# Performance work log

Measured on AMD Instinct MI355X. Metric: run time of the kernel, lower is better.

Reference implementation:

```python
import jax, jax.numpy as jnp
import numpy as np

V, H, TS, TT, B, PAD = 32000, 512, 48, 48, 64, 0


def setup_inputs() -> dict:
    key = jax.random.key(0)
    ks = jax.random.split(key, 26)
    s = 0.02
    rn = lambda k, shape: (jax.random.normal(k, shape, jnp.float32) * s)
    emb = rn(ks[0], (V, H)).at[PAD].set(0.0)  # padding_idx row zeroed
    return dict(
        src=jax.random.randint(ks[1], (TS, B), 0, V),
        tgt=jax.random.randint(ks[2], (TT, B), 0, V),
        emb=emb,
        enc0_Wih=rn(ks[3], (3 * H, H)), enc0_bih=rn(ks[4], (3 * H,)),
        enc0_Ur=rn(ks[5], (H, H)), enc0_Uz=rn(ks[6], (H, H)),
        enc0_Un=rn(ks[7], (H, H)), enc0_bn=rn(ks[8], (H,)),
        enc1_Wih=rn(ks[9], (3 * H, 2 * H)), enc1_bih=rn(ks[10], (3 * H,)),
        enc1_Ur=rn(ks[11], (H, H)), enc1_Uz=rn(ks[12], (H, H)),
        enc1_Un=rn(ks[13], (H, H)), enc1_bn=rn(ks[14], (H,)),
        fc_init_w=rn(ks[15], (H, 2 * H)), fc_init_b=rn(ks[16], (H,)),
        Wa=rn(ks[17], (2 * H, H)),
        attn_combine_w=rn(ks[18], (H, 3 * H)),
        dec_Wih=rn(ks[19], (3 * H, 2 * H)), dec_bih=rn(ks[20], (3 * H,)),
        dec_Ur=rn(ks[21], (H, H)), dec_Uz=rn(ks[22], (H, H)),
        dec_Un=rn(ks[23], (H, H)), dec_bn=rn(ks[24], (H,)),
        out_w=rn(ks[25], (V, H)),
    )


def _gru_step(xp, h, Ur, Uz, Un, bn):
    # xp: (B, 3H) pre-projected input; h: (B, H)
    rx, zx, nx = jnp.split(xp, 3, axis=-1)
    r = jax.nn.sigmoid(rx + h @ Ur.T)
    z = jax.nn.sigmoid(zx + h @ Uz.T)
    n = jnp.tanh(nx + r * (h @ Un.T + bn))
    return (1.0 - z) * n + z * h


def _bigru_layer(x, Wih, bih, Ur, Uz, Un, bn):
    # x: (T, B, in). W_ih applied once for both directions (shared).
    Bb = x.shape[1]
    Hh = Ur.shape[0]
    xp = x @ Wih.T + bih  # (T, B, 3H)
    def step(h, xpt):
        h2 = _gru_step(xpt, h, Ur, Uz, Un, bn)
        return h2, h2
    h0 = jnp.zeros((Bb, Hh), x.dtype)
    hf, fwd = jax.lax.scan(step, h0, xp)
    hb, bwd = jax.lax.scan(step, h0, xp[::-1])
    out = jnp.concatenate([fwd, bwd[::-1]], axis=-1)  # (T, B, 2H)
    return out, hf, hb


def reference(src, tgt, emb,
              enc0_Wih, enc0_bih, enc0_Ur, enc0_Uz, enc0_Un, enc0_bn,
              enc1_Wih, enc1_bih, enc1_Ur, enc1_Uz, enc1_Un, enc1_bn,
              fc_init_w, fc_init_b, Wa, attn_combine_w,
              dec_Wih, dec_bih, dec_Ur, dec_Uz, dec_Un, dec_bn, out_w):
    Hh = dec_Ur.shape[0]
    Bb = src.shape[1]
    # ---- encode (direction='en_de' -> transpose_U=False; dropout = eval/identity) ----
    x = emb[src]                                           # (Ts, B, H)
    l0, _, _ = _bigru_layer(x, enc0_Wih, enc0_bih, enc0_Ur, enc0_Uz, enc0_Un, enc0_bn)
    H_enc, hf, hb = _bigru_layer(l0, enc1_Wih, enc1_bih, enc1_Ur, enc1_Uz, enc1_Un, enc1_bn)
    h0 = jnp.tanh(jnp.concatenate([hf, hb], axis=-1) @ fc_init_w.T + fc_init_b)
    src_mask = (src == PAD).T                              # (B, Ts)
    Henc_b = jnp.transpose(H_enc, (1, 0, 2))               # (B, Ts, 2H)
    scale = 1.0 / np.sqrt(2 * Hh).astype(np.float32)
    # ---- decode ----
    tgt_emb = emb[tgt]                                     # (Tt, B, H)
    ht0 = jnp.zeros((Bb, Hh), jnp.float32)
    def dec_step(carry, x_t):
        h, ht = carry
        gin = jnp.concatenate([x_t, ht], axis=-1)          # (B, 2H)
        xp = gin @ dec_Wih.T + dec_bih
        h = _gru_step(xp, h, dec_Ur, dec_Uz, dec_Un, dec_bn)
        q = h @ Wa.T                                       # (B, 2H)
        scores = jnp.einsum('bd,btd->bt', q, Henc_b) * scale
        scores = jnp.where(src_mask, jnp.float32(-1e9), scores)
        alpha = jax.nn.softmax(scores, axis=1)
        ctx = jnp.einsum('bt,btd->bd', alpha, Henc_b)      # (B, 2H)
        ht = jnp.tanh(jnp.concatenate([h, ctx], axis=-1) @ attn_combine_w.T)
        logits = ht @ out_w.T                              # (B, V)
        return (h, ht), logits
    _, logits = jax.lax.scan(dec_step, (h0, ht0), tgt_emb)
    return logits                                          # (Tt, B, V)
```

## Files before the change

kernel.cpp:

```cpp
#include <hip/hip_runtime.h>
#include <math.h>

#define TSE 48
#define TTD 48
#define BB  64
#define HH  512
#define VV  32000

__device__ __forceinline__ float sigmoidf_(float x) { return 1.0f / (1.0f + expf(-x)); }

__global__ __launch_bounds__(256) void zero_f32(float* __restrict__ p, int n) {
    int i = blockIdx.x * 256 + threadIdx.x;
    if (i < n) p[i] = 0.0f;
}

__global__ __launch_bounds__(128) void gather_emb(const int* __restrict__ idx,
                                                  const float* __restrict__ emb,
                                                  float* __restrict__ out) {
    int row = blockIdx.x;
    int v = idx[row];
    const float4* s = (const float4*)(emb + (size_t)v * HH);
    float4* d = (float4*)(out + (size_t)row * HH);
    d[threadIdx.x] = s[threadIdx.x];
}

template <int TRANSB, int BIAS>
__global__ __launch_bounds__(256) void gemm_f32(const float* __restrict__ A,
                                                const float* __restrict__ Bm,
                                                const float* __restrict__ bias,
                                                float* __restrict__ C,
                                                int M, int N, int K, int lda, int ldb, int ldc) {
    __shared__ float As[32][132];
    __shared__ float Bs[32][132];
    const int tid = threadIdx.x;
    const int tx = tid & 15, ty = tid >> 4;
    const int m0 = blockIdx.y * 128, n0 = blockIdx.x * 128;

    float acc[8][8];
#pragma unroll
    for (int i = 0; i < 8; i++)
#pragma unroll
        for (int j = 0; j < 8; j++) acc[i][j] = 0.0f;

    const int arow = tid >> 1, akq = (tid & 1) * 16;
    const int bk = tid >> 3, bnq = (tid & 7) * 16;

    for (int k0 = 0; k0 < K; k0 += 32) {
        float4 av[4], bv[4];
        const float* ap = A + (size_t)(m0 + arow) * lda + k0 + akq;
#pragma unroll
        for (int q = 0; q < 4; q++) av[q] = *(const float4*)(ap + 4 * q);
        if (TRANSB) {
            const float* bp = Bm + (size_t)(n0 + arow) * ldb + k0 + akq;
#pragma unroll
            for (int q = 0; q < 4; q++) bv[q] = *(const float4*)(bp + 4 * q);
        } else {
            const float* bp = Bm + (size_t)(k0 + bk) * ldb + n0 + bnq;
#pragma unroll
            for (int q = 0; q < 4; q++) bv[q] = *(const float4*)(bp + 4 * q);
        }
        __syncthreads();
#pragma unroll
        for (int q = 0; q < 4; q++) {
            As[akq + 4 * q + 0][arow] = av[q].x;
            As[akq + 4 * q + 1][arow] = av[q].y;
            As[akq + 4 * q + 2][arow] = av[q].z;
            As[akq + 4 * q + 3][arow] = av[q].w;
        }
        if (TRANSB) {
#pragma unroll
            for (int q = 0; q < 4; q++) {
                Bs[akq + 4 * q + 0][arow] = bv[q].x;
                Bs[akq + 4 * q + 1][arow] = bv[q].y;
                Bs[akq + 4 * q + 2][arow] = bv[q].z;
                Bs[akq + 4 * q + 3][arow] = bv[q].w;
            }
        } else {
#pragma unroll
            for (int q = 0; q < 4; q++) *(float4*)&Bs[bk][bnq + 4 * q] = bv[q];
        }
        __syncthreads();
#pragma unroll
        for (int kk = 0; kk < 32; kk++) {
            float4 a0 = *(const float4*)&As[kk][ty * 8];
            float4 a1 = *(const float4*)&As[kk][ty * 8 + 4];
            float4 b0 = *(const float4*)&Bs[kk][tx * 8];
            float4 b1 = *(const float4*)&Bs[kk][tx * 8 + 4];
            float aa[8] = {a0.x, a0.y, a0.z, a0.w, a1.x, a1.y, a1.z, a1.w};
            float bb[8] = {b0.x, b0.y, b0.z, b0.w, b1.x, b1.y, b1.z, b1.w};
#pragma unroll
            for (int i = 0; i < 8; i++)
#pragma unroll
                for (int j = 0; j < 8; j++) acc[i][j] += aa[i] * bb[j];
        }
    }

    float bb8[8];
#pragma unroll
    for (int j = 0; j < 8; j++) bb8[j] = BIAS ? bias[n0 + tx * 8 + j] : 0.0f;
#pragma unroll
    for (int i = 0; i < 8; i++) {
        float* cp = C + (size_t)(m0 + ty * 8 + i) * ldc + n0 + tx * 8;
        float4 v0 = {acc[i][0] + bb8[0], acc[i][1] + bb8[1], acc[i][2] + bb8[2], acc[i][3] + bb8[3]};
        float4 v1 = {acc[i][4] + bb8[4], acc[i][5] + bb8[5], acc[i][6] + bb8[6], acc[i][7] + bb8[7]};
        *(float4*)cp = v0;
        *(float4*)(cp + 4) = v1;
    }
}

__global__ __launch_bounds__(256) void enc_gru_step(const float* __restrict__ xp,
                                                    const float* __restrict__ Ur,
                                                    const float* __restrict__ Uz,
                                                    const float* __restrict__ Un,
                                                    const float* __restrict__ bn,
                                                    const float* __restrict__ hprev,
                                                    float* __restrict__ hnew,
                                                    float* __restrict__ outbuf, int s) {
    const int bid = blockIdx.x;
    const int dir = bid >> 7;
    const int bt = (bid >> 4) & 7;
    const int jt = bid & 15;
    const int j = jt * 32 + (threadIdx.x & 31);
    const int b = bt * 8 + (threadIdx.x >> 5);
    const int t = dir ? (TSE - 1 - s) : s;
    const float* hp = hprev + ((size_t)((dir << 6) + b)) * HH;
    const float* ur = Ur + (size_t)j * HH;
    const float* uz = Uz + (size_t)j * HH;
    const float* un = Un + (size_t)j * HH;
    float ar = 0.f, az = 0.f, an = 0.f;
#pragma unroll 4
    for (int k = 0; k < HH; k += 4) {
        float4 h4 = *(const float4*)(hp + k);
        float4 r4 = *(const float4*)(ur + k);
        float4 z4 = *(const float4*)(uz + k);
        float4 n4 = *(const float4*)(un + k);
        ar += h4.x * r4.x + h4.y * r4.y + h4.z * r4.z + h4.w * r4.w;
        az += h4.x * z4.x + h4.y * z4.y + h4.z * z4.z + h4.w * z4.w;
        an += h4.x * n4.x + h4.y * n4.y + h4.z * n4.z + h4.w * n4.w;
    }
    const float* xpt = xp + ((size_t)t * BB + b) * 1536;
    float r = sigmoidf_(xpt[j] + ar);
    float z = sigmoidf_(xpt[512 + j] + az);
    float n = tanhf(xpt[1024 + j] + r * (an + bn[j]));
    float hv = hp[j];
    float hn = (1.f - z) * n + z * hv;
    hnew[((size_t)((dir << 6) + b)) * HH + j] = hn;
    outbuf[((size_t)t * BB + b) * 1024 + (dir << 9) + j] = hn;
}

__global__ __launch_bounds__(256) void dec_gru_step(const float* __restrict__ xpx,
                                                    const float* __restrict__ Wih,
                                                    const float* __restrict__ Ur,
                                                    const float* __restrict__ Uz,
                                                    const float* __restrict__ Un,
                                                    const float* __restrict__ bn,
                                                    const float* __restrict__ htprev,
                                                    const float* __restrict__ hprev,
                                                    float* __restrict__ hnew, int t) {
    const int bid = blockIdx.x;
    const int bt = bid >> 4, jt = bid & 15;
    const int j = jt * 32 + (threadIdx.x & 31);
    const int b = bt * 8 + (threadIdx.x >> 5);
    const float* hp = hprev + (size_t)b * HH;
    const float* qp = htprev + (size_t)b * HH;
    const float* ur = Ur + (size_t)j * HH;
    const float* uz = Uz + (size_t)j * HH;
    const float* un = Un + (size_t)j * HH;
    const float* wr = Wih + (size_t)j * 1024 + 512;
    const float* wz = Wih + (size_t)(512 + j) * 1024 + 512;
    const float* wn = Wih + (size_t)(1024 + j) * 1024 + 512;
    float ar = 0.f, az = 0.f, an = 0.f, xr = 0.f, xz = 0.f, xn = 0.f;
#pragma unroll 2
    for (int k = 0; k < HH; k += 4) {
        float4 h4 = *(const float4*)(hp + k);
        float4 q4 = *(const float4*)(qp + k);
        float4 r4 = *(const float4*)(ur + k);
        float4 z4 = *(const float4*)(uz + k);
        float4 n4 = *(const float4*)(un + k);
        float4 a4 = *(const float4*)(wr + k);
        float4 b4 = *(const float4*)(wz + k);
        float4 c4 = *(const float4*)(wn + k);
        ar += h4.x * r4.x + h4.y * r4.y + h4.z * r4.z + h4.w * r4.w;
        az += h4.x * z4.x + h4.y * z4.y + h4.z * z4.z + h4.w * z4.w;
        an += h4.x * n4.x + h4.y * n4.y + h4.z * n4.z + h4.w * n4.w;
        xr += q4.x * a4.x + q4.y * a4.y + q4.z * a4.z + q4.w * a4.w;
        xz += q4.x * b4.x + q4.y * b4.y + q4.z * b4.z + q4.w * b4.w;
        xn += q4.x * c4.x + q4.y * c4.y + q4.z * c4.z + q4.w * c4.w;
    }
    const float* xpt = xpx + ((size_t)t * BB + b) * 1536;
    float r = sigmoidf_(xpt[j] + xr + ar);
    float z = sigmoidf_(xpt[512 + j] + xz + az);
    float n = tanhf(xpt[1024 + j] + xn + r * (an + bn[j]));
    float hv = hp[j];
    hnew[(size_t)b * HH + j] = (1.f - z) * n + z * hv;
}

__global__ __launch_bounds__(256) void attn_step(const float* __restrict__ h,
                                                 const float* __restrict__ Katt,
                                                 const float* __restrict__ Henc,
                                                 const int* __restrict__ src,
                                                 float* __restrict__ ctx) {
    const int b = blockIdx.x;
    const int tid = threadIdx.x;
    const int lane = tid & 63, w = tid >> 6;
    __shared__ float sc[TSE];
    const float* hb = h + (size_t)b * HH;
    const float4* hp4 = (const float4*)(hb + lane * 8);
    float4 hv0 = hp4[0], hv1 = hp4[1];
    for (int tt = w; tt < TSE; tt += 4) {
        const float4* kp4 = (const float4*)(Katt + ((size_t)tt * BB + b) * HH + lane * 8);
        float4 k0 = kp4[0], k1 = kp4[1];
        float s = k0.x * hv0.x + k0.y * hv0.y + k0.z * hv0.z + k0.w * hv0.w +
                  k1.x * hv1.x + k1.y * hv1.y + k1.z * hv1.z + k1.w * hv1.w;
#pragma unroll
        for (int off = 32; off; off >>= 1) s += __shfl_down(s, off);
        if (lane == 0) {
            float val = s * 0.03125f;
            if (src[tt * BB + b] == 0) val = -1e9f;
            sc[tt] = val;
        }
    }
    __syncthreads();
    if (tid < 64) {
        float v = (tid < TSE) ? sc[tid] : -3.0e38f;
        float m = v;
#pragma unroll
        for (int off = 32; off; off >>= 1) m = fmaxf(m, __shfl_xor(m, off));
        float e = (tid < TSE) ? expf(v - m) : 0.f;
        float ssum = e;
#pragma unroll
        for (int off = 32; off; off >>= 1) ssum += __shfl_xor(ssum, off);
        if (tid < TSE) sc[tid] = e / ssum;
    }
    __syncthreads();
    for (int d = tid; d < 1024; d += 256) {
        float acc = 0.f;
#pragma unroll 4
        for (int tt = 0; tt < TSE; ++tt) acc += sc[tt] * Henc[((size_t)tt * BB + b) * 1024 + d];
        ctx[(size_t)b * 1024 + d] = acc;
    }
}

__global__ __launch_bounds__(256) void combine_step(const float* __restrict__ h,
                                                    const float* __restrict__ ctx,
                                                    const float* __restrict__ Wc,
                                                    float* __restrict__ ht_out) {
    const int bid = blockIdx.x;
    const int bt = bid >> 4, jt = bid & 15;
    const int j = jt * 32 + (threadIdx.x & 31);
    const int b = bt * 8 + (threadIdx.x >> 5);
    const float* hb = h + (size_t)b * HH;
    const float* cb = ctx + (size_t)b * 1024;
    const float* w0 = Wc + (size_t)j * 1536;
    float acc = 0.f;
#pragma unroll 4
    for (int k = 0; k < 512; k += 4) {
        float4 h4 = *(const float4*)(hb + k);
        float4 w4 = *(const float4*)(w0 + k);
        acc += h4.x * w4.x + h4.y * w4.y + h4.z * w4.z + h4.w * w4.w;
    }
#pragma unroll 4
    for (int k = 0; k < 1024; k += 4) {
        float4 c4 = *(const float4*)(cb + k);
        float4 w4 = *(const float4*)(w0 + 512 + k);
        acc += c4.x * w4.x + c4.y * w4.y + c4.z * w4.z + c4.w * w4.w;
    }
    ht_out[(size_t)b * HH + j] = tanhf(acc);
}

__global__ __launch_bounds__(256) void fc_init_k(const float* __restrict__ hf,
                                                 const float* __restrict__ hb,
                                                 const float* __restrict__ W,
                                                 const float* __restrict__ bias,
                                                 float* __restrict__ h0) {
    const int bid = blockIdx.x;
    const int bt = bid >> 4, jt = bid & 15;
    const int j = jt * 32 + (threadIdx.x & 31);
    const int b = bt * 8 + (threadIdx.x >> 5);
    const float* w0 = W + (size_t)j * 1024;
    float acc = bias[j];
#pragma unroll 4
    for (int k = 0; k < 512; k += 4) {
        float4 h4 = *(const float4*)(hf + (size_t)b * HH + k);
        float4 w4 = *(const float4*)(w0 + k);
        acc += h4.x * w4.x + h4.y * w4.y + h4.z * w4.z + h4.w * w4.w;
    }
#pragma unroll 4
    for (int k = 0; k < 512; k += 4) {
        float4 h4 = *(const float4*)(hb + (size_t)b * HH + k);
        float4 w4 = *(const float4*)(w0 + 512 + k);
        acc += h4.x * w4.x + h4.y * w4.y + h4.z * w4.z + h4.w * w4.w;
    }
    h0[(size_t)b * HH + j] = tanhf(acc);
}

extern "C" void kernel_launch(void* const* d_in, const int* in_sizes, int n_in,
                              void* d_out, int out_size, void* d_ws, size_t ws_size,
                              hipStream_t stream) {
    const int* src = (const int*)d_in[0];
    const int* tgt = (const int*)d_in[1];
    const float* emb = (const float*)d_in[2];
    const float* e0Wih = (const float*)d_in[3];
    const float* e0bih = (const float*)d_in[4];
    const float* e0Ur = (const float*)d_in[5];
    const float* e0Uz = (const float*)d_in[6];
    const float* e0Un = (const float*)d_in[7];
    const float* e0bn = (const float*)d_in[8];
    const float* e1Wih = (const float*)d_in[9];
    const float* e1bih = (const float*)d_in[10];
    const float* e1Ur = (const float*)d_in[11];
    const float* e1Uz = (const float*)d_in[12];
    const float* e1Un = (const float*)d_in[13];
    const float* e1bn = (const float*)d_in[14];
    const float* fcW = (const float*)d_in[15];
    const float* fcB = (const float*)d_in[16];
    const float* Wa = (const float*)d_in[17];
    const float* Wc = (const float*)d_in[18];
    const float* dWih = (const float*)d_in[19];
    const float* dbih = (const float*)d_in[20];
    const float* dUr = (const float*)d_in[21];
    const float* dUz = (const float*)d_in[22];
    const float* dUn = (const float*)d_in[23];
    const float* dbn = (const float*)d_in[24];
    const float* outW = (const float*)d_in[25];
    float* out = (float*)d_out;
    float* w = (float*)d_ws;

    float* x_buf = w;
    float* xp01 = w + 1572864;
    float* l0 = w + 6291456;
    float* Henc = w + 9437184;
    float* xp_x = w + 12582912;
    float* ht_all = w + 17301504;
    float* enc_h = w + 18874368;
    float* dec_h = w + 19005440;
    float* ht_zero = w + 19070976;
    float* ctx = w + 19103744;
    if (ws_size < (size_t)19169280 * 4) return;

    zero_f32<<<256, 256, 0, stream>>>(enc_h, 65536);
    zero_f32<<<128, 256, 0, stream>>>(ht_zero, 32768);

    gather_emb<<<3072, 128, 0, stream>>>(src, emb, x_buf);
    (gemm_f32<1, 1>)<<<dim3(12, 24), 256, 0, stream>>>(x_buf, e0Wih, e0bih, xp01,
                                                       3072, 1536, 512, 512, 512, 1536);
    for (int s = 0; s < TSE; s++)
        enc_gru_step<<<256, 256, 0, stream>>>(xp01, e0Ur, e0Uz, e0Un, e0bn,
                                              enc_h + (s & 1) * 65536,
                                              enc_h + ((s + 1) & 1) * 65536, l0, s);
    gather_emb<<<3072, 128, 0, stream>>>(tgt, emb, x_buf);
    (gemm_f32<1, 1>)<<<dim3(12, 24), 256, 0, stream>>>(l0, e1Wih, e1bih, xp01,
                                                       3072, 1536, 1024, 1024, 1024, 1536);
    zero_f32<<<256, 256, 0, stream>>>(enc_h, 65536);
    for (int s = 0; s < TSE; s++)
        enc_gru_step<<<256, 256, 0, stream>>>(xp01, e1Ur, e1Uz, e1Un, e1bn,
                                              enc_h + (s & 1) * 65536,
                                              enc_h + ((s + 1) & 1) * 65536, Henc, s);
    fc_init_k<<<128, 256, 0, stream>>>(enc_h, enc_h + 32768, fcW, fcB, dec_h);

    (gemm_f32<0, 0>)<<<dim3(4, 24), 256, 0, stream>>>(Henc, Wa, nullptr, l0,
                                                      3072, 512, 1024, 1024, 512, 512);
    (gemm_f32<1, 1>)<<<dim3(12, 24), 256, 0, stream>>>(x_buf, dWih, dbih, xp_x,
                                                       3072, 1536, 512, 512, 1024, 1536);

    for (int t = 0; t < TTD; t++) {
        const float* htp = (t == 0) ? ht_zero : (ht_all + (size_t)(t - 1) * 32768);
        float* hcur = dec_h + (t & 1) * 32768;
        float* hnext = dec_h + ((t + 1) & 1) * 32768;
        dec_gru_step<<<128, 256, 0, stream>>>(xp_x, dWih, dUr, dUz, dUn, dbn, htp, hcur, hnext, t);
        attn_step<<<64, 256, 0, stream>>>(hnext, l0, Henc, src, ctx);
        combine_step<<<128, 256, 0, stream>>>(hnext, ctx, Wc, ht_all + (size_t)t * 32768);
    }

    (gemm_f32<1, 0>)<<<dim3(250, 24), 256, 0, stream>>>(ht_all, outW, nullptr, out,
                                                        3072, 32000, 512, 512, 512, 32000);
}
```

Measured before the change: 15.28 ms.

## Use split-bf16 MFMA GEMMs for input projections and output logits

Adds an MFMA GEMM that emulates fp32 precision by splitting each operand into bf16 hi and lo parts and summing three bf16 products. The large output projection and the input-projection GEMMs move from the scalar fp32 tiled GEMM onto matrix cores. Operands are converted each call by new split kernels, which adds extra memory traffic, notably on the 32000x512 output weight. The path only runs when the workspace is large enough, otherwise it falls back to the old code.

```diff
diff --git a/kernel.cpp b/kernel.cpp
--- a/kernel.cpp
+++ b/kernel.cpp
@@ -8,6 +8,16 @@
 #define VV  32000
 
 __device__ __forceinline__ float sigmoidf_(float x) { return 1.0f / (1.0f + expf(-x)); }
+
+__device__ __forceinline__ ushort f2bf(float x) {
+    uint u = __float_as_uint(x);
+    u += 0x7FFF + ((u >> 16) & 1);
+    return (ushort)(u >> 16);
+}
+__device__ __forceinline__ float bf2f(ushort h) { return __uint_as_float(((uint)h) << 16); }
+
+typedef __attribute__((ext_vector_type(8))) __bf16 bf16x8;
+typedef __attribute__((ext_vector_type(4))) float f32x4;
 
 __global__ __launch_bounds__(256) void zero_f32(float* __restrict__ p, int n) {
     int i = blockIdx.x * 256 + threadIdx.x;
@@ -22,6 +32,112 @@
     const float4* s = (const float4*)(emb + (size_t)v * HH);
     float4* d = (float4*)(out + (size_t)row * HH);
     d[threadIdx.x] = s[threadIdx.x];
+}
+
+__global__ __launch_bounds__(256) void split4(const float* __restrict__ in,
+                                              ushort* __restrict__ hi, ushort* __restrict__ lo, int n) {
+    int i = (blockIdx.x * 256 + threadIdx.x) * 4;
+    if (i >= n) return;
+    float4 v = *(const float4*)(in + i);
+    ushort h0 = f2bf(v.x), h1 = f2bf(v.y), h2 = f2bf(v.z), h3 = f2bf(v.w);
+    ushort4 H = {h0, h1, h2, h3};
+    ushort4 L = {f2bf(v.x - bf2f(h0)), f2bf(v.y - bf2f(h1)), f2bf(v.z - bf2f(h2)), f2bf(v.w - bf2f(h3))};
+    *(ushort4*)(hi + i) = H;
+    *(ushort4*)(lo + i) = L;
+}
+
+__global__ __launch_bounds__(256) void split4_dwx(const float* __restrict__ in,
+                                                  ushort* __restrict__ hi, ushort* __restrict__ lo, int n) {
+    int i = (blockIdx.x * 256 + threadIdx.x) * 4;
+    if (i >= n) return;
+    int r = i >> 9, c = i & 511;
+    float4 v = *(const float4*)(in + (size_t)r * 1024 + c);
+    ushort h0 = f2bf(v.x), h1 = f2bf(v.y), h2 = f2bf(v.z), h3 = f2bf(v.w);
+    ushort4 H = {h0, h1, h2, h3};
+    ushort4 L = {f2bf(v.x - bf2f(h0)), f2bf(v.y - bf2f(h1)), f2bf(v.z - bf2f(h2)), f2bf(v.w - bf2f(h3))};
+    *(ushort4*)(hi + i) = H;
+    *(ushort4*)(lo + i) = L;
+}
+
+__global__ __launch_bounds__(256) void split_waT(const float* __restrict__ Wa,
+                                                 ushort* __restrict__ hi, ushort* __restrict__ lo) {
+    int o = blockIdx.x * 256 + threadIdx.x;
+    int e = o >> 10, d = o & 1023;
+    float v = Wa[(size_t)d * 512 + e];
+    ushort h = f2bf(v);
+    hi[o] = h;
+    lo[o] = f2bf(v - bf2f(h));
+}
+
+template <int BIAS>
+__global__ __launch_bounds__(256, 2) void gemm_mfma(const ushort* __restrict__ Ahi,
+                                                    const ushort* __restrict__ Alo,
+                                                    const ushort* __restrict__ Bhi,
+                                                    const ushort* __restrict__ Blo,
+                                                    const float* __restrict__ bias,
+                                                    float* __restrict__ C,
+                                                    int K, int ldc) {
+    __shared__ ushort sA[2][128 * 32];
+    __shared__ ushort sB[2][128 * 32];
+    const int tid = threadIdx.x;
+    const int wid = tid >> 6, lane = tid & 63;
+    const int m0 = blockIdx.y << 7, n0 = blockIdx.x << 7;
+
+    const ushort* gb;
+    ushort* lb;
+    switch (wid) {
+        case 0: gb = Ahi + (size_t)m0 * K; lb = sA[0]; break;
+        case 1: gb = Alo + (size_t)m0 * K; lb = sA[1]; break;
+        case 2: gb = Bhi + (size_t)n0 * K; lb = sB[0]; break;
+        default: gb = Blo + (size_t)n0 * K; lb = sB[1]; break;
+    }
+    gb += (size_t)(lane >> 2) * K + (lane & 3) * 8;
+
+    const int wr = (wid >> 1) << 6, wc = (wid & 1) << 6;
+    const int frow = lane & 15, fk = (lane >> 4) << 3;
+    f32x4 acc[4][4];
+#pragma unroll
+    for (int i = 0; i < 4; i++)
+#pragma unroll
+        for (int j = 0; j < 4; j++) acc[i][j] = (f32x4){0.f, 0.f, 0.f, 0.f};
+
+    for (int k0 = 0; k0 < K; k0 += 32) {
+        __syncthreads();
+#pragma unroll
+        for (int c = 0; c < 8; ++c)
+            __builtin_amdgcn_global_load_lds(
+                (const __attribute__((address_space(1))) void*)(gb + k0 + (size_t)(c << 4) * K),
+                (__attribute__((address_space(3))) void*)(lb + (c << 9)), 16, 0, 0);
+        __syncthreads();
+        bf16x8 ah[4], al[4], bh[4], bl[4];
+#pragma unroll
+        for (int i = 0; i < 4; ++i) {
+            ah[i] = *(const bf16x8*)&sA[0][((wr + (i << 4) + frow) << 5) + fk];
+            al[i] = *(const bf16x8*)&sA[1][((wr + (i << 4) + frow) << 5) + fk];
+            bh[i] = *(const bf16x8*)&sB[0][((wc + (i << 4) + frow) << 5) + fk];
+            bl[i] = *(const bf16x8*)&sB[1][((wc + (i << 4) + frow) << 5) + fk];
+        }
+#pragma unroll
+        for (int i = 0; i < 4; ++i)
+#pragma unroll
+            for (int j = 0; j < 4; ++j) {
+                acc[i][j] = __builtin_amdgcn_mfma_f32_16x16x32_bf16(ah[i], bh[j], acc[i][j], 0, 0, 0);
+                acc[i][j] = __builtin_amdgcn_mfma_f32_16x16x32_bf16(al[i], bh[j], acc[i][j], 0, 0, 0);
+                acc[i][j] = __builtin_amdgcn_mfma_f32_16x16x32_bf16(ah[i], bl[j], acc[i][j], 0, 0, 0);
+            }
+    }
+    const int crow = (lane >> 4) << 2, ccol = lane & 15;
+#pragma unroll
+    for (int j = 0; j < 4; ++j) {
+        int n = n0 + wc + (j << 4) + ccol;
+        float bv = BIAS ? bias[n] : 0.f;
+#pragma unroll
+        for (int i = 0; i < 4; ++i) {
+            float* cp = C + (size_t)(m0 + wr + (i << 4) + crow) * ldc + n;
+#pragma unroll
+            for (int r = 0; r < 4; ++r) cp[(size_t)r * ldc] = acc[i][j][r] + bv;
+        }
+    }
 }
 
 template <int TRANSB, int BIAS>
@@ -341,37 +457,95 @@
     zero_f32<<<256, 256, 0, stream>>>(enc_h, 65536);
     zero_f32<<<128, 256, 0, stream>>>(ht_zero, 32768);
 
-    gather_emb<<<3072, 128, 0, stream>>>(src, emb, x_buf);
-    (gemm_f32<1, 1>)<<<dim3(12, 24), 256, 0, stream>>>(x_buf, e0Wih, e0bih, xp01,
-                                                       3072, 1536, 512, 512, 512, 1536);
-    for (int s = 0; s < TSE; s++)
-        enc_gru_step<<<256, 256, 0, stream>>>(xp01, e0Ur, e0Uz, e0Un, e0bn,
-                                              enc_h + (s & 1) * 65536,
-                                              enc_h + ((s + 1) & 1) * 65536, l0, s);
-    gather_emb<<<3072, 128, 0, stream>>>(tgt, emb, x_buf);
-    (gemm_f32<1, 1>)<<<dim3(12, 24), 256, 0, stream>>>(l0, e1Wih, e1bih, xp01,
-                                                       3072, 1536, 1024, 1024, 1024, 1536);
-    zero_f32<<<256, 256, 0, stream>>>(enc_h, 65536);
-    for (int s = 0; s < TSE; s++)
-        enc_gru_step<<<256, 256, 0, stream>>>(xp01, e1Ur, e1Uz, e1Un, e1bn,
-                                              enc_h + (s & 1) * 65536,
-                                              enc_h + ((s + 1) & 1) * 65536, Henc, s);
-    fc_init_k<<<128, 256, 0, stream>>>(enc_h, enc_h + 32768, fcW, fcB, dec_h);
-
-    (gemm_f32<0, 0>)<<<dim3(4, 24), 256, 0, stream>>>(Henc, Wa, nullptr, l0,
-                                                      3072, 512, 1024, 1024, 512, 512);
-    (gemm_f32<1, 1>)<<<dim3(12, 24), 256, 0, stream>>>(x_buf, dWih, dbih, xp_x,
-                                                       3072, 1536, 512, 512, 1024, 1536);
-
-    for (int t = 0; t < TTD; t++) {
-        const float* htp = (t == 0) ? ht_zero : (ht_all + (size_t)(t - 1) * 32768);
-        float* hcur = dec_h + (t & 1) * 32768;
-        float* hnext = dec_h + ((t + 1) & 1) * 32768;
-        dec_gru_step<<<128, 256, 0, stream>>>(xp_x, dWih, dUr, dUz, dUn, dbn, htp, hcur, hnext, t);
-        attn_step<<<64, 256, 0, stream>>>(hnext, l0, Henc, src, ctx);
-        combine_step<<<128, 256, 0, stream>>>(hnext, ctx, Wc, ht_all + (size_t)t * 32768);
-    }
-
-    (gemm_f32<1, 0>)<<<dim3(250, 24), 256, 0, stream>>>(ht_all, outW, nullptr, out,
-                                                        3072, 32000, 512, 512, 512, 32000);
-}
+    const bool use_mfma = ws_size >= (size_t)103940096;
+
+    if (use_mfma) {
+        ushort* u = (ushort*)(w + 19169280);
+        ushort* e0hi = u;
+        ushort* e0lo = u + 786432;
+        ushort* e1hi = u + 1572864;
+        ushort* e1lo = u + 3145728;
+        ushort* wahi = u + 4718592;
+        ushort* walo = u + 5242880;
+        ushort* dxhi = u + 5767168;
+        ushort* dxlo = u + 6553600;
+        ushort* Ahi = u + 7340032;
+        ushort* Alo = u + 10485760;
+
+        split4<<<768, 256, 0, stream>>>(e0Wih, e0hi, e0lo, 786432);
+        split4<<<1536, 256, 0, stream>>>(e1Wih, e1hi, e1lo, 1572864);
+        split_waT<<<2048, 256, 0, stream>>>(Wa, wahi, walo);
+        split4_dwx<<<768, 256, 0, stream>>>(dWih, dxhi, dxlo, 786432);
+
+        gather_emb<<<3072, 128, 0, stream>>>(src, emb, x_buf);
+        split4<<<1536, 256, 0, stream>>>(x_buf, Ahi, Alo, 1572864);
+        (gemm_mfma<1>)<<<dim3(12, 24), 256, 0, stream>>>(Ahi, Alo, e0hi, e0lo, e0bih, xp01, 512, 1536);
+        for (int s = 0; s < TSE; s++)
+            enc_gru_step<<<256, 256, 0, stream>>>(xp01, e0Ur, e0Uz, e0Un, e0bn,
+                                                  enc_h + (s & 1) * 65536,
+                                                  enc_h + ((s + 1) & 1) * 65536, l0, s);
+        gather_emb<<<3072, 128, 0, stream>>>(tgt, emb, x_buf);
+        split4<<<3072, 256, 0, stream>>>(l0, Ahi, Alo, 3145728);
+        (gemm_mfma<1>)<<<dim3(12, 24), 256, 0, stream>>>(Ahi, Alo, e1hi, e1lo, e1bih, xp01, 1024, 1536);
+        zero_f32<<<256, 256, 0, stream>>>(enc_h, 65536);
+        for (int s = 0; s < TSE; s++)
+            enc_gru_step<<<256, 256, 0, stream>>>(xp01, e1Ur, e1Uz, e1Un, e1bn,
+                                                  enc_h + (s & 1) * 65536,
+                                                  enc_h + ((s + 1) & 1) * 65536, Henc, s);
+        fc_init_k<<<128, 256, 0, stream>>>(enc_h, enc_h + 32768, fcW, fcB, dec_h);
+
+        split4<<<3072, 256, 0, stream>>>(Henc, Ahi, Alo, 3145728);
+        (gemm_mfma<0>)<<<dim3(4, 24), 256, 0, stream>>>(Ahi, Alo, wahi, walo, nullptr, l0, 1024, 512);
+        split4<<<1536, 256, 0, stream>>>(x_buf, Ahi, Alo, 1572864);
+        (gemm_mfma<1>)<<<dim3(12, 24), 256, 0, stream>>>(Ahi, Alo, dxhi, dxlo, dbih, xp_x, 512, 1536);
+
+        for (int t = 0; t < TTD; t++) {
+            const float* htp = (t == 0) ? ht_zero : (ht_all + (size_t)(t - 1) * 32768);
+            float* hcur = dec_h + (t & 1) * 32768;
+            float* hnext = dec_h + ((t + 1) & 1) * 32768;
+            dec_gru_step<<<128, 256, 0, stream>>>(xp_x, dWih, dUr, dUz, dUn, dbn, htp, hcur, hnext, t);
+            attn_step<<<64, 256, 0, stream>>>(hnext, l0, Henc, src, ctx);
+            combine_step<<<128, 256, 0, stream>>>(hnext, ctx, Wc, ht_all + (size_t)t * 32768);
+        }
+
+        ushort* oWhi = (ushort*)w;
+        ushort* oWlo = (ushort*)(w + 8192000);
+        split4<<<16000, 256, 0, stream>>>(outW, oWhi, oWlo, 16384000);
+        split4<<<1536, 256, 0, stream>>>(ht_all, Ahi, Alo, 1572864);
+        (gemm_mfma<0>)<<<dim3(250, 24), 256, 0, stream>>>(Ahi, Alo, oWhi, oWlo, nullptr, out, 512, 32000);
+    } else {
+        gather_emb<<<3072, 128, 0, stream>>>(src, emb, x_buf);
+        (gemm_f32<1, 1>)<<<dim3(12, 24), 256, 0, stream>>>(x_buf, e0Wih, e0bih, xp01,
+                                                           3072, 1536, 512, 512, 512, 1536);
+        for (int s = 0; s < TSE; s++)
+            enc_gru_step<<<256, 256, 0, stream>>>(xp01, e0Ur, e0Uz, e0Un, e0bn,
+                                                  enc_h + (s & 1) * 65536,
+                                                  enc_h + ((s + 1) & 1) * 65536, l0, s);
+        gather_emb<<<3072, 128, 0, stream>>>(tgt, emb, x_buf);
+        (gemm_f32<1, 1>)<<<dim3(12, 24), 256, 0, stream>>>(l0, e1Wih, e1bih, xp01,
+                                                           3072, 1536, 1024, 1024, 1024, 1536);
+        zero_f32<<<256, 256, 0, stream>>>(enc_h, 65536);
+        for (int s = 0; s < TSE; s++)
+            enc_gru_step<<<256, 256, 0, stream>>>(xp01, e1Ur, e1Uz, e1Un, e1bn,
+                                                  enc_h + (s & 1) * 65536,
+                                                  enc_h + ((s + 1) & 1) * 65536, Henc, s);
+        fc_init_k<<<128, 256, 0, stream>>>(enc_h, enc_h + 32768, fcW, fcB, dec_h);
+
+        (gemm_f32<0, 0>)<<<dim3(4, 24), 256, 0, stream>>>(Henc, Wa, nullptr, l0,
+                                                          3072, 512, 1024, 1024, 512, 512);
+        (gemm_f32<1, 1>)<<<dim3(12, 24), 256, 0, stream>>>(x_buf, dWih, dbih, xp_x,
+                                                           3072, 1536, 512, 512, 1024, 1536);
+
+        for (int t = 0; t < TTD; t++) {
+            const float* htp = (t == 0) ? ht_zero : (ht_all + (size_t)(t - 1) * 32768);
+            float* hcur = dec_h + (t & 1) * 32768;
+            float* hnext = dec_h + ((t + 1) & 1) * 32768;
+            dec_gru_step<<<128, 256, 0, stream>>>(xp_x, dWih, dUr, dUz, dUn, dbn, htp, hcur, hnext, t);
+            attn_step<<<64, 256, 0, stream>>>(hnext, l0, Henc, src, ctx);
+            combine_step<<<128, 256, 0, stream>>>(hnext, ctx, Wc, ht_all + (size_t)t * 32768);
+        }
+
+        (gemm_f32<1, 0>)<<<dim3(250, 24), 256, 0, stream>>>(ht_all, outW, nullptr, out,
+                                                            3072, 32000, 512, 512, 512, 32000);
+    }
+}
```

Measured after the change: 14.19 ms. -7.1%, faster.
